# Kernel tuning notes

Hardware: AMD Instinct MI355X
Metric: run time of the kernel (lower is better)

Reference implementation:

```python
import jax, jax.numpy as jnp
import numpy as np

EPS = 0.001
NUM_HEAD = 4

def _bn(x, g, b, m, v):
    # x: [B,C,H,W]; per-channel affine batchnorm in eval mode
    inv = g / jnp.sqrt(v + EPS)
    return x * inv[None, :, None, None] + (b - m * inv)[None, :, None, None]

def setup_inputs() -> dict:
    key = jax.random.key(0)
    ks = jax.random.split(key, 16)
    B, C, H, W = 8, 256, 40, 40
    C2 = 2 * C
    return {
        "x": jax.random.normal(ks[0], (B, C, H, W), jnp.float32),
        "qkv_w": jax.random.normal(ks[1], (C2, C), jnp.float32) * 0.05,
        "qkv_g": jax.random.uniform(ks[2], (C2,), jnp.float32),
        "qkv_b": jax.random.normal(ks[3], (C2,), jnp.float32) * 0.05,
        "qkv_m": jax.random.normal(ks[4], (C2,), jnp.float32) * 0.05,
        "qkv_v": jax.random.uniform(ks[5], (C2,), jnp.float32) + 0.5,
        "cb1_w": jax.random.normal(ks[6], (C, 1, 3, 3), jnp.float32) * 0.05,
        "cb1_g": jax.random.uniform(ks[7], (C,), jnp.float32),
        "cb1_b": jax.random.normal(ks[8], (C,), jnp.float32) * 0.05,
        "cb1_m": jax.random.normal(ks[9], (C,), jnp.float32) * 0.05,
        "cb1_v": jax.random.uniform(ks[10], (C,), jnp.float32) + 0.5,
        "cb2_w": jax.random.normal(ks[11], (C, C), jnp.float32) * 0.05,
        "cb2_g": jax.random.uniform(ks[12], (C,), jnp.float32),
        "cb2_b": jax.random.normal(ks[13], (C,), jnp.float32) * 0.05,
        "cb2_m": jax.random.normal(ks[14], (C,), jnp.float32) * 0.05,
        "cb2_v": jax.random.uniform(ks[15], (C,), jnp.float32) + 0.5,
    }

def reference(x, qkv_w, qkv_g, qkv_b, qkv_m, qkv_v,
              cb1_w, cb1_g, cb1_b, cb1_m, cb1_v,
              cb2_w, cb2_g, cb2_b, cb2_m, cb2_v):
    B, C, H, W = x.shape
    nh = NUM_HEAD
    dh = C // nh          # dim_head
    dk = dh // 2          # dim_key
    scale = dk ** -0.5
    L = H * W

    # qkv: 1x1 conv (ch -> 2ch) + BN
    qkv = jnp.einsum('oc,bchw->bohw', qkv_w, x)
    qkv = _bn(qkv, qkv_g, qkv_b, qkv_m, qkv_v)
    qkv = qkv.reshape(B, nh, 2 * dk + dh, L)
    q, k, v = qkv[:, :, :dk], qkv[:, :, dk:2 * dk], qkv[:, :, 2 * dk:]

    # attn = q^T @ k * scale -> softmax over last dim
    attn = jnp.einsum('bndq,bndk->bnqk', q, k) * scale  # [B,nh,L,L]
    attn = jax.nn.softmax(attn, axis=-1)

    # y = v @ attn^T : y[d,q] = sum_k v[d,k] * attn[q,k]
    y = jnp.einsum('bndk,bnqk->bndq', v, attn).reshape(B, C, H, W)

    # depthwise 3x3 conv branch on v + BN
    vr = v.reshape(B, C, H, W)
    dw = jax.lax.conv_general_dilated(
        vr, cb1_w, window_strides=(1, 1), padding=((1, 1), (1, 1)),
        feature_group_count=C, dimension_numbers=('NCHW', 'OIHW', 'NCHW'))
    y = y + _bn(dw, cb1_g, cb1_b, cb1_m, cb1_v)

    # final 1x1 conv + BN
    out = jnp.einsum('oc,bchw->bohw', cb2_w, y)
    return _bn(out, cb2_g, cb2_b, cb2_m, cb2_v)
```

## Files before the change

kernel.cpp:

```cpp
#include <hip/hip_runtime.h>
#include <hip/hip_bf16.h>

#define EPS 1e-3f
#define QSC_LOG2E 0.2550348653f

typedef __attribute__((ext_vector_type(8))) short bf16x8;
typedef __attribute__((ext_vector_type(4))) float f32x4;
typedef __attribute__((ext_vector_type(4))) unsigned short u16x4;
typedef __attribute__((ext_vector_type(8))) unsigned short u16x8;
typedef __attribute__((ext_vector_type(2))) unsigned int u32x2;

typedef const __attribute__((address_space(1))) unsigned int g_u32;
typedef __attribute__((address_space(3))) unsigned int l_u32;

__device__ __forceinline__ unsigned short f2bf(float f) {
    union { float f; unsigned u; } v; v.f = f;
    unsigned r = v.u + 0x7FFFu + ((v.u >> 16) & 1u);
    return (unsigned short)(r >> 16);
}
__device__ __forceinline__ float bf2f(unsigned short h) {
    union { unsigned u; float f; } v; v.u = ((unsigned)h) << 16;
    return v.f;
}
__device__ __forceinline__ unsigned pkbf(float lo, float hi) {
    float2 t; t.x = lo; t.y = hi;
    __hip_bfloat162 h = __float22bfloat162_rn(t);
    union { __hip_bfloat162 h; unsigned u; } c; c.h = h;
    return c.u;
}

__global__ __launch_bounds__(256) void conv_kernel(
    const float* __restrict__ wq, const float* __restrict__ wc,
    unsigned short* __restrict__ wqb, unsigned short* __restrict__ wcb,
    const float* __restrict__ x, unsigned short* __restrict__ xt)
{
    int bid = blockIdx.x;
    int tid = threadIdx.x;
    if (bid < 192) {
        int i = (bid * 256 + tid) * 4;
        const float* src; unsigned short* dst; int off;
        if (i < 131072) { src = wq; dst = wqb; off = i; }
        else            { src = wc; dst = wcb; off = i - 131072; }
        f32x4 v = *(const f32x4*)(src + off);
        u16x4 o;
        #pragma unroll
        for (int j = 0; j < 4; ++j) o[j] = f2bf(v[j]);
        *(u16x4*)(dst + off) = o;
        return;
    }
    __shared__ float t[64][65];
    int bid2 = bid - 192;
    int l0 = (bid2 % 25) * 64, c0 = ((bid2 / 25) & 3) * 64, b = bid2 / 100;
    const float* xb = x + ((size_t)b * 256 + c0) * 1600 + l0;
    #pragma unroll
    for (int p = 0; p < 4; ++p) {
        int row = p * 16 + (tid >> 4);
        int col = (tid & 15) * 4;
        f32x4 v = *(const f32x4*)(xb + (size_t)row * 1600 + col);
        #pragma unroll
        for (int j = 0; j < 4; ++j) t[row][col + j] = v[j];
    }
    __syncthreads();
    int l = tid >> 2, cs = tid & 3;
    u16x8 o0, o1;
    #pragma unroll
    for (int i = 0; i < 8; ++i) o0[i] = f2bf(t[cs * 16 + i][l]);
    #pragma unroll
    for (int i = 0; i < 8; ++i) o1[i] = f2bf(t[cs * 16 + 8 + i][l]);
    unsigned short* dst = xt + ((size_t)b * 1600 + l0 + l) * 256 + c0 + cs * 16;
    *(u16x8*)dst = o0;
    *(u16x8*)(dst + 8) = o1;
}

__global__ __launch_bounds__(256) void qkv_gemm_kernel(
    const unsigned short* __restrict__ wqb, const unsigned short* __restrict__ xt,
    const float* __restrict__ gg, const float* __restrict__ bet,
    const float* __restrict__ mm, const float* __restrict__ vv,
    unsigned short* __restrict__ qk, unsigned short* __restrict__ vt,
    unsigned short* __restrict__ v2)
{
    __shared__ unsigned short ldsT[4][32 * 72];

    const int tid = threadIdx.x, wid = tid >> 6, lane = tid & 63;
    const int g = lane >> 4, cc = lane & 15;
    const int gl0 = blockIdx.x * 128 + (wid & 1) * 64;
    const int o_base = blockIdx.y * 64 + (wid >> 1) * 32;

    const unsigned short* wb0 = wqb + (size_t)(o_base + cc) * 256;
    const unsigned short* wb1 = wqb + (size_t)(o_base + 16 + cc) * 256;
    const unsigned short* xb  = xt + (size_t)(gl0 + cc) * 256;

    const f32x4 fz = {0.f, 0.f, 0.f, 0.f};
    f32x4 acc[2][4] = {{fz, fz, fz, fz}, {fz, fz, fz, fz}};
    #pragma unroll 4
    for (int kk = 0; kk < 256; kk += 32) {
        bf16x8 a0 = *(const bf16x8*)(wb0 + kk + 8 * g);
        bf16x8 a1 = *(const bf16x8*)(wb1 + kk + 8 * g);
        #pragma unroll
        for (int f = 0; f < 4; ++f) {
            bf16x8 bfr = *(const bf16x8*)(xb + (size_t)f * 16 * 256 + kk + 8 * g);
            acc[0][f] = __builtin_amdgcn_mfma_f32_16x16x32_bf16(a0, bfr, acc[0][f], 0, 0, 0);
            acc[1][f] = __builtin_amdgcn_mfma_f32_16x16x32_bf16(a1, bfr, acc[1][f], 0, 0, 0);
        }
    }

    const int head = blockIdx.y >> 1;
    const bool is_v = blockIdx.y & 1;
    float inv[2][4], bias[2][4];
    #pragma unroll
    for (int i = 0; i < 2; ++i) {
        #pragma unroll
        for (int r = 0; r < 4; ++r) {
            int oc = o_base + 16 * i + 4 * g + r;
            float iv = gg[oc] * rsqrtf(vv[oc] + EPS);
            float bs = bet[oc] - mm[oc] * iv;
            if ((oc & 127) < 32) { iv *= QSC_LOG2E; bs *= QSC_LOG2E; }
            inv[i][r] = iv; bias[i][r] = bs;
        }
    }

    if (!is_v) {
        #pragma unroll
        for (int f = 0; f < 4; ++f) {
            int gl = gl0 + 16 * f + cc;
            int b  = gl / 1600;
            int ll = gl - b * 1600;
            unsigned short* dst = qk + ((size_t)(b * 4 + head) * 1600 + ll) * 64;
            #pragma unroll
            for (int i = 0; i < 2; ++i) {
                u16x4 pk;
                #pragma unroll
                for (int r = 0; r < 4; ++r) pk[r] = f2bf(acc[i][f][r] * inv[i][r] + bias[i][r]);
                *(u16x4*)(dst + (o_base & 63) + 16 * i + 4 * g) = pk;
            }
        }
    } else {
        const int d_base = (o_base & 63);
        #pragma unroll
        for (int f = 0; f < 4; ++f) {
            int gl = gl0 + 16 * f + cc;
            unsigned short* v2dst = v2 + (size_t)gl * 256 + head * 64 + d_base;
            #pragma unroll
            for (int i = 0; i < 2; ++i) {
                u16x4 pk;
                #pragma unroll
                for (int r = 0; r < 4; ++r) {
                    unsigned short h = f2bf(acc[i][f][r] * inv[i][r] + bias[i][r]);
                    pk[r] = h;
                    ldsT[wid][(16 * i + 4 * g + r) * 72 + 16 * f + cc] = h;
                }
                *(u16x4*)(v2dst + 16 * i + 4 * g) = pk;
            }
        }
        asm volatile("s_waitcnt lgkmcnt(0)" ::: "memory");
        #pragma unroll
        for (int j = 0; j < 4; ++j) {
            int p = j * 64 + lane;
            int d_loc = p >> 3, c8 = p & 7;
            u16x8 val = *(const u16x8*)&ldsT[wid][d_loc * 72 + c8 * 8];
            int gl_c = gl0 + c8 * 8;
            int b  = gl_c / 1600;
            int ll = gl_c - b * 1600;
            *(u16x8*)(vt + ((size_t)(b * 4 + head) * 64 + d_base + d_loc) * 1600 + ll) = val;
        }
    }
}

__global__ __launch_bounds__(256) void attn_kernel(
    const unsigned short* __restrict__ qk, const unsigned short* __restrict__ vt,
    unsigned short* __restrict__ y_t)
{
    __shared__ __align__(16) unsigned short kbuf[2][64 * 32];
    __shared__ __align__(16) unsigned short vbuf[2][64 * 64];

    const int tid = threadIdx.x, wid = tid >> 6, lane = tid & 63;
    const int g = lane >> 4, cc = lane & 15;
    const int pair = blockIdx.x;
    const int q0 = blockIdx.y * 64 + wid * 16;

    const unsigned short* qkb = qk + (size_t)pair * 1600 * 64;
    const unsigned short* vtb = vt + (size_t)pair * 64 * 1600;

    bf16x8 bq = *(const bf16x8*)(qkb + (size_t)(q0 + cc) * 64 + 8 * g);

    const int krow = tid >> 2, kchk = tid & 3;
    const unsigned short* kP = qkb + (size_t)krow * 64 + 32 + (kchk ^ (krow & 3)) * 8;
    const int vrow = tid >> 3, vchk = tid & 7;
    const unsigned short* vPa = vtb + (size_t)vrow * 1600 + (vchk ^ (vrow & 7)) * 8;
    const unsigned short* vPb = vPa + (size_t)32 * 1600;

    const unsigned short* kr0  = &kbuf[0][cc * 32 + (g ^ (cc & 3)) * 8];
    const unsigned short* kr1  = &kbuf[1][cc * 32 + (g ^ (cc & 3)) * 8];
    const unsigned short* vr0a = &vbuf[0][cc * 64 + ((g) ^ (cc & 7)) * 8];
    const unsigned short* vr0b = &vbuf[0][cc * 64 + ((4 + g) ^ (cc & 7)) * 8];
    const unsigned short* vr1a = &vbuf[1][cc * 64 + ((g) ^ (cc & 7)) * 8];
    const unsigned short* vr1b = &vbuf[1][cc * 64 + ((4 + g) ^ (cc & 7)) * 8];

    #define STAGE(bufi)                                                               \
        do {                                                                          \
            __builtin_amdgcn_global_load_lds((g_u32*)kP,                              \
                (l_u32*)(&kbuf[bufi][wid * 512]), 16, 0, 0);                          \
            __builtin_amdgcn_global_load_lds((g_u32*)vPa,                             \
                (l_u32*)(&vbuf[bufi][wid * 512]), 16, 0, 0);                          \
            __builtin_amdgcn_global_load_lds((g_u32*)vPb,                             \
                (l_u32*)(&vbuf[bufi][2048 + wid * 512]), 16, 0, 0);                   \
            kP += 4096; vPa += 64; vPb += 64;                                         \
        } while (0)

    const f32x4 fz = {0.f, 0.f, 0.f, 0.f};
    const short one_bf = (short)0x3F80;
    const bf16x8 ones = {one_bf, one_bf, one_bf, one_bf, one_bf, one_bf, one_bf, one_bf};
    f32x4 o[4] = {fz, fz, fz, fz};
    f32x4 sumacc = fz;

    auto compute = [&](const unsigned short* kr, const unsigned short* vra,
                       const unsigned short* vrb) {
        bf16x8 kf[4], vf[8];
        #pragma unroll
        for (int f = 0; f < 4; ++f)
            kf[f] = *(const bf16x8*)(kr + f * 512);
        #pragma unroll
        for (int f2 = 0; f2 < 4; ++f2) {
            vf[2 * f2]     = *(const bf16x8*)(vra + f2 * 1024);
            vf[2 * f2 + 1] = *(const bf16x8*)(vrb + f2 * 1024);
        }

        f32x4 s4[4];
        __builtin_amdgcn_s_setprio(1);
        #pragma unroll
        for (int f = 0; f < 4; ++f)
            s4[f] = __builtin_amdgcn_mfma_f32_16x16x32_bf16(kf[f], bq, fz, 0, 0, 0);
        __builtin_amdgcn_s_setprio(0);

        unsigned c2[4][2];
        #pragma unroll
        for (int f = 0; f < 4; ++f) {
            float p0 = exp2f(s4[f][0]), p1 = exp2f(s4[f][1]);
            float p2 = exp2f(s4[f][2]), p3 = exp2f(s4[f][3]);
            c2[f][0] = pkbf(p0, p1);
            c2[f][1] = pkbf(p2, p3);
        }
        unsigned pb_u[2][4];
        #pragma unroll
        for (int s2 = 0; s2 < 2; ++s2) {
            const int fA = 2 * s2, fB = 2 * s2 + 1;
            u32x2 xy0 = __builtin_amdgcn_permlane32_swap(c2[fA][0], c2[fB][0], false, false);
            u32x2 xy1 = __builtin_amdgcn_permlane32_swap(c2[fA][1], c2[fB][1], false, false);
            u32x2 w02 = __builtin_amdgcn_permlane16_swap(xy0.x, xy0.y, false, false);
            u32x2 w13 = __builtin_amdgcn_permlane16_swap(xy1.x, xy1.y, false, false);
            pb_u[s2][0] = w02.x;
            pb_u[s2][1] = w13.x;
            pb_u[s2][2] = w02.y;
            pb_u[s2][3] = w13.y;
        }

        __builtin_amdgcn_s_setprio(1);
        #pragma unroll
        for (int s2 = 0; s2 < 2; ++s2) {
            union { unsigned u[4]; bf16x8 v; } pb;
            #pragma unroll
            for (int j = 0; j < 4; ++j) pb.u[j] = pb_u[s2][j];
            #pragma unroll
            for (int f2 = 0; f2 < 4; ++f2)
                o[f2] = __builtin_amdgcn_mfma_f32_16x16x32_bf16(vf[f2 * 2 + s2], pb.v, o[f2], 0, 0, 0);
            sumacc = __builtin_amdgcn_mfma_f32_16x16x32_bf16(ones, pb.v, sumacc, 0, 0, 0);
        }
        __builtin_amdgcn_s_setprio(0);
    };

    STAGE(0);
    __syncthreads();

    for (int j = 0; j < 12; ++j) {
        STAGE(1);
        compute(kr0, vr0a, vr0b);
        __syncthreads();
        STAGE(0);
        compute(kr1, vr1a, vr1b);
        __syncthreads();
    }
    compute(kr0, vr0a, vr0b);
    #undef STAGE

    float il = 1.f / sumacc[0];
    const int n = pair & 3, b = pair >> 2;
    unsigned short* yb = y_t + ((size_t)b * 1600 + q0 + cc) * 256 + n * 64;
    #pragma unroll
    for (int f2 = 0; f2 < 4; ++f2) {
        u16x4 st;
        #pragma unroll
        for (int r = 0; r < 4; ++r) st[r] = f2bf(o[f2][r] * il);
        *(u16x4*)(yb + 16 * f2 + 4 * g) = st;
    }
}

__global__ __launch_bounds__(256) void dw_kernel(
    const unsigned short* __restrict__ v2, unsigned short* __restrict__ y_t,
    const float* __restrict__ cw, const float* __restrict__ gg,
    const float* __restrict__ bet, const float* __restrict__ mm,
    const float* __restrict__ vv)
{
    const int tid = threadIdx.x;
    const int gl = blockIdx.x * 64 + (tid & 63);
    const int c0 = blockIdx.y * 32 + (tid >> 6) * 8;
    const int b = gl / 1600;
    const int l = gl - b * 1600;
    const int h = l / 40, w = l - h * 40;

    float s[8];
    #pragma unroll
    for (int i = 0; i < 8; ++i) s[i] = 0.f;
    #pragma unroll
    for (int kh = -1; kh <= 1; ++kh) {
        int hh = h + kh;
        if (hh < 0 || hh >= 40) continue;
        #pragma unroll
        for (int kw = -1; kw <= 1; ++kw) {
            int ww = w + kw;
            if (ww < 0 || ww >= 40) continue;
            u16x8 vv8 = *(const u16x8*)(v2 + (size_t)(gl + kh * 40 + kw) * 256 + c0);
            const int tap = (kh + 1) * 3 + (kw + 1);
            #pragma unroll
            for (int i = 0; i < 8; ++i)
                s[i] = fmaf(bf2f(vv8[i]), cw[(c0 + i) * 9 + tap], s[i]);
        }
    }
    u16x8 yv = *(const u16x8*)(y_t + (size_t)gl * 256 + c0);
    u16x8 out;
    #pragma unroll
    for (int i = 0; i < 8; ++i) {
        int c = c0 + i;
        float iv = gg[c] * rsqrtf(vv[c] + EPS);
        out[i] = f2bf(bf2f(yv[i]) + s[i] * iv + (bet[c] - mm[c] * iv));
    }
    *(u16x8*)(y_t + (size_t)gl * 256 + c0) = out;
}

__global__ __launch_bounds__(256) void out_gemm_kernel(
    const unsigned short* __restrict__ wcb, const unsigned short* __restrict__ y_t,
    const float* __restrict__ gg, const float* __restrict__ bet,
    const float* __restrict__ mm, const float* __restrict__ vv,
    float* __restrict__ out)
{
    const int tid = threadIdx.x, wid = tid >> 6, lane = tid & 63;
    const int g = lane >> 4, cc = lane & 15;
    const int gl0 = blockIdx.x * 128 + (wid & 1) * 64;
    const int o_base = blockIdx.y * 64 + (wid >> 1) * 32;

    const unsigned short* wb0 = wcb + (size_t)(o_base + cc) * 256;
    const unsigned short* wb1 = wcb + (size_t)(o_base + 16 + cc) * 256;
    const unsigned short* yb  = y_t + (size_t)(gl0 + cc) * 256;

    const f32x4 fz = {0.f, 0.f, 0.f, 0.f};
    f32x4 acc[2][4] = {{fz, fz, fz, fz}, {fz, fz, fz, fz}};
    #pragma unroll 4
    for (int kk = 0; kk < 256; kk += 32) {
        bf16x8 a0 = *(const bf16x8*)(wb0 + kk + 8 * g);
        bf16x8 a1 = *(const bf16x8*)(wb1 + kk + 8 * g);
        #pragma unroll
        for (int f = 0; f < 4; ++f) {
            bf16x8 bfr = *(const bf16x8*)(yb + (size_t)f * 16 * 256 + kk + 8 * g);
            acc[0][f] = __builtin_amdgcn_mfma_f32_16x16x32_bf16(a0, bfr, acc[0][f], 0, 0, 0);
            acc[1][f] = __builtin_amdgcn_mfma_f32_16x16x32_bf16(a1, bfr, acc[1][f], 0, 0, 0);
        }
    }
    #pragma unroll
    for (int i = 0; i < 2; ++i) {
        #pragma unroll
        for (int r = 0; r < 4; ++r) {
            int oc = o_base + 16 * i + 4 * g + r;
            float iv = gg[oc] * rsqrtf(vv[oc] + EPS);
            float bs = bet[oc] - mm[oc] * iv;
            #pragma unroll
            for (int f = 0; f < 4; ++f) {
                int gl = gl0 + 16 * f + cc;
                int b  = gl / 1600;
                int ll = gl - b * 1600;
                out[((size_t)b * 256 + oc) * 1600 + ll] = acc[i][f][r] * iv + bs;
            }
        }
    }
}

extern "C" void kernel_launch(void* const* d_in, const int* in_sizes, int n_in,
                              void* d_out, int out_size, void* d_ws, size_t ws_size,
                              hipStream_t stream) {
    const float* x     = (const float*)d_in[0];
    const float* qkv_w = (const float*)d_in[1];
    const float* qkv_g = (const float*)d_in[2];
    const float* qkv_b = (const float*)d_in[3];
    const float* qkv_m = (const float*)d_in[4];
    const float* qkv_v = (const float*)d_in[5];
    const float* cb1_w = (const float*)d_in[6];
    const float* cb1_g = (const float*)d_in[7];
    const float* cb1_b = (const float*)d_in[8];
    const float* cb1_m = (const float*)d_in[9];
    const float* cb1_v = (const float*)d_in[10];
    const float* cb2_w = (const float*)d_in[11];
    const float* cb2_g = (const float*)d_in[12];
    const float* cb2_b = (const float*)d_in[13];
    const float* cb2_m = (const float*)d_in[14];
    const float* cb2_v = (const float*)d_in[15];
    float* out = (float*)d_out;

    unsigned short* ws16 = (unsigned short*)d_ws;
    const size_t N16 = 3276800;
    unsigned short* xt  = ws16;
    unsigned short* qk  = ws16 + N16;
    unsigned short* vt  = ws16 + 2 * N16;
    unsigned short* y_t = ws16 + 3 * N16;
    unsigned short* v2  = ws16 + 4 * N16;
    unsigned short* wqb = ws16 + 5 * N16;
    unsigned short* wcb = wqb + 131072;

    conv_kernel<<<dim3(992), 256, 0, stream>>>(qkv_w, cb2_w, wqb, wcb, x, xt);
    qkv_gemm_kernel<<<dim3(100, 8), 256, 0, stream>>>(wqb, xt, qkv_g, qkv_b, qkv_m, qkv_v, qk, vt, v2);
    attn_kernel<<<dim3(32, 25), 256, 0, stream>>>(qk, vt, y_t);
    dw_kernel<<<dim3(200, 8), 256, 0, stream>>>(v2, y_t, cb1_w, cb1_g, cb1_b, cb1_m, cb1_v);
    out_gemm_kernel<<<dim3(100, 4), 256, 0, stream>>>(wcb, y_t, cb2_g, cb2_b, cb2_m, cb2_v, out);
}
```

Before: 118.7 us.

## Fuse depthwise conv into output GEMM via LDS and relax attention barriers

Merges the depthwise 3x3 conv + BN kernel with the final 1x1 conv GEMM. Each block computes 32 positions of the combined y into shared memory, then runs the MFMA GEMM across all 256 output channels. This drops one launch and the round trip of y_t through global memory. Separately, the attention loop's __syncthreads are replaced by explicit s_waitcnt vmcnt(3) plus raw barriers so prefetched loads can stay in flight across the barrier. The cost is a smaller grid (400 blocks), repeated weight reads per block, and a hand-tuned vmcnt that must match the number of loads STAGE issues.

```diff
diff --git a/kernel.cpp b/kernel.cpp
--- a/kernel.cpp
+++ b/kernel.cpp
@@ -269,16 +269,21 @@
     };
 
     STAGE(0);
-    __syncthreads();
 
     for (int j = 0; j < 12; ++j) {
         STAGE(1);
+        asm volatile("s_waitcnt vmcnt(3)" ::: "memory");
+        __builtin_amdgcn_s_barrier();
         compute(kr0, vr0a, vr0b);
-        __syncthreads();
+        __builtin_amdgcn_s_barrier();
         STAGE(0);
+        asm volatile("s_waitcnt vmcnt(3)" ::: "memory");
+        __builtin_amdgcn_s_barrier();
         compute(kr1, vr1a, vr1b);
-        __syncthreads();
-    }
+        __builtin_amdgcn_s_barrier();
+    }
+    asm volatile("s_waitcnt vmcnt(0)" ::: "memory");
+    __builtin_amdgcn_s_barrier();
     compute(kr0, vr0a, vr0b);
     #undef STAGE
 
@@ -294,85 +299,90 @@
     }
 }
 
-__global__ __launch_bounds__(256) void dw_kernel(
-    const unsigned short* __restrict__ v2, unsigned short* __restrict__ y_t,
-    const float* __restrict__ cw, const float* __restrict__ gg,
-    const float* __restrict__ bet, const float* __restrict__ mm,
-    const float* __restrict__ vv)
-{
-    const int tid = threadIdx.x;
-    const int gl = blockIdx.x * 64 + (tid & 63);
-    const int c0 = blockIdx.y * 32 + (tid >> 6) * 8;
-    const int b = gl / 1600;
-    const int l = gl - b * 1600;
-    const int h = l / 40, w = l - h * 40;
-
-    float s[8];
-    #pragma unroll
-    for (int i = 0; i < 8; ++i) s[i] = 0.f;
-    #pragma unroll
-    for (int kh = -1; kh <= 1; ++kh) {
-        int hh = h + kh;
-        if (hh < 0 || hh >= 40) continue;
-        #pragma unroll
-        for (int kw = -1; kw <= 1; ++kw) {
-            int ww = w + kw;
-            if (ww < 0 || ww >= 40) continue;
-            u16x8 vv8 = *(const u16x8*)(v2 + (size_t)(gl + kh * 40 + kw) * 256 + c0);
-            const int tap = (kh + 1) * 3 + (kw + 1);
-            #pragma unroll
-            for (int i = 0; i < 8; ++i)
-                s[i] = fmaf(bf2f(vv8[i]), cw[(c0 + i) * 9 + tap], s[i]);
-        }
-    }
-    u16x8 yv = *(const u16x8*)(y_t + (size_t)gl * 256 + c0);
-    u16x8 out;
-    #pragma unroll
-    for (int i = 0; i < 8; ++i) {
-        int c = c0 + i;
-        float iv = gg[c] * rsqrtf(vv[c] + EPS);
-        out[i] = f2bf(bf2f(yv[i]) + s[i] * iv + (bet[c] - mm[c] * iv));
-    }
-    *(u16x8*)(y_t + (size_t)gl * 256 + c0) = out;
-}
-
-__global__ __launch_bounds__(256) void out_gemm_kernel(
-    const unsigned short* __restrict__ wcb, const unsigned short* __restrict__ y_t,
-    const float* __restrict__ gg, const float* __restrict__ bet,
-    const float* __restrict__ mm, const float* __restrict__ vv,
+__global__ __launch_bounds__(256) void dwout_kernel(
+    const unsigned short* __restrict__ v2, const unsigned short* __restrict__ y_t,
+    const float* __restrict__ cw, const float* __restrict__ g1,
+    const float* __restrict__ b1, const float* __restrict__ m1,
+    const float* __restrict__ v1,
+    const unsigned short* __restrict__ wcb, const float* __restrict__ g2,
+    const float* __restrict__ b2, const float* __restrict__ m2,
+    const float* __restrict__ vbn2,
     float* __restrict__ out)
 {
+    __shared__ unsigned short y2s[32][264];
+
     const int tid = threadIdx.x, wid = tid >> 6, lane = tid & 63;
     const int g = lane >> 4, cc = lane & 15;
-    const int gl0 = blockIdx.x * 128 + (wid & 1) * 64;
-    const int o_base = blockIdx.y * 64 + (wid >> 1) * 32;
-
-    const unsigned short* wb0 = wcb + (size_t)(o_base + cc) * 256;
-    const unsigned short* wb1 = wcb + (size_t)(o_base + 16 + cc) * 256;
-    const unsigned short* yb  = y_t + (size_t)(gl0 + cc) * 256;
+    const int gl0 = blockIdx.x * 32;
+
+    {
+        const int gl_loc = tid & 31, cpart = tid >> 5;
+        const int gl = gl0 + gl_loc;
+        const int b = gl / 1600, l = gl - b * 1600;
+        const int h = l / 40, w = l - h * 40;
+        #pragma unroll
+        for (int cg = 0; cg < 4; ++cg) {
+            const int c0 = cpart * 32 + cg * 8;
+            float s[8];
+            #pragma unroll
+            for (int i = 0; i < 8; ++i) s[i] = 0.f;
+            #pragma unroll
+            for (int kh = -1; kh <= 1; ++kh) {
+                int hh = h + kh;
+                if (hh < 0 || hh >= 40) continue;
+                #pragma unroll
+                for (int kw = -1; kw <= 1; ++kw) {
+                    int ww = w + kw;
+                    if (ww < 0 || ww >= 40) continue;
+                    u16x8 vv8 = *(const u16x8*)(v2 + (size_t)(gl + kh * 40 + kw) * 256 + c0);
+                    const int tap = (kh + 1) * 3 + (kw + 1);
+                    #pragma unroll
+                    for (int i = 0; i < 8; ++i)
+                        s[i] = fmaf(bf2f(vv8[i]), cw[(c0 + i) * 9 + tap], s[i]);
+                }
+            }
+            u16x8 yv = *(const u16x8*)(y_t + (size_t)gl * 256 + c0);
+            u16x8 o8;
+            #pragma unroll
+            for (int i = 0; i < 8; ++i) {
+                int c = c0 + i;
+                float iv = g1[c] * rsqrtf(v1[c] + EPS);
+                o8[i] = f2bf(bf2f(yv[i]) + s[i] * iv + (b1[c] - m1[c] * iv));
+            }
+            *(u16x8*)&y2s[gl_loc][c0] = o8;
+        }
+    }
+    __syncthreads();
+
+    const int o_base = wid * 64;
+    const unsigned short* wb = wcb + (size_t)(o_base + cc) * 256;
 
     const f32x4 fz = {0.f, 0.f, 0.f, 0.f};
-    f32x4 acc[2][4] = {{fz, fz, fz, fz}, {fz, fz, fz, fz}};
+    f32x4 acc[4][2] = {{fz, fz}, {fz, fz}, {fz, fz}, {fz, fz}};
     #pragma unroll 4
     for (int kk = 0; kk < 256; kk += 32) {
-        bf16x8 a0 = *(const bf16x8*)(wb0 + kk + 8 * g);
-        bf16x8 a1 = *(const bf16x8*)(wb1 + kk + 8 * g);
-        #pragma unroll
-        for (int f = 0; f < 4; ++f) {
-            bf16x8 bfr = *(const bf16x8*)(yb + (size_t)f * 16 * 256 + kk + 8 * g);
-            acc[0][f] = __builtin_amdgcn_mfma_f32_16x16x32_bf16(a0, bfr, acc[0][f], 0, 0, 0);
-            acc[1][f] = __builtin_amdgcn_mfma_f32_16x16x32_bf16(a1, bfr, acc[1][f], 0, 0, 0);
-        }
-    }
-    #pragma unroll
-    for (int i = 0; i < 2; ++i) {
+        bf16x8 a[4], bfr[2];
+        #pragma unroll
+        for (int i = 0; i < 4; ++i)
+            a[i] = *(const bf16x8*)(wb + (size_t)i * 16 * 256 + kk + 8 * g);
+        #pragma unroll
+        for (int f = 0; f < 2; ++f)
+            bfr[f] = *(const bf16x8*)&y2s[16 * f + cc][kk + 8 * g];
+        #pragma unroll
+        for (int i = 0; i < 4; ++i)
+            #pragma unroll
+            for (int f = 0; f < 2; ++f)
+                acc[i][f] = __builtin_amdgcn_mfma_f32_16x16x32_bf16(a[i], bfr[f], acc[i][f], 0, 0, 0);
+    }
+    #pragma unroll
+    for (int i = 0; i < 4; ++i) {
         #pragma unroll
         for (int r = 0; r < 4; ++r) {
             int oc = o_base + 16 * i + 4 * g + r;
-            float iv = gg[oc] * rsqrtf(vv[oc] + EPS);
-            float bs = bet[oc] - mm[oc] * iv;
-            #pragma unroll
-            for (int f = 0; f < 4; ++f) {
+            float iv = g2[oc] * rsqrtf(vbn2[oc] + EPS);
+            float bs = b2[oc] - m2[oc] * iv;
+            #pragma unroll
+            for (int f = 0; f < 2; ++f) {
                 int gl = gl0 + 16 * f + cc;
                 int b  = gl / 1600;
                 int ll = gl - b * 1600;
@@ -416,6 +426,6 @@
     conv_kernel<<<dim3(992), 256, 0, stream>>>(qkv_w, cb2_w, wqb, wcb, x, xt);
     qkv_gemm_kernel<<<dim3(100, 8), 256, 0, stream>>>(wqb, xt, qkv_g, qkv_b, qkv_m, qkv_v, qk, vt, v2);
     attn_kernel<<<dim3(32, 25), 256, 0, stream>>>(qk, vt, y_t);
-    dw_kernel<<<dim3(200, 8), 256, 0, stream>>>(v2, y_t, cb1_w, cb1_g, cb1_b, cb1_m, cb1_v);
-    out_gemm_kernel<<<dim3(100, 4), 256, 0, stream>>>(wcb, y_t, cb2_g, cb2_b, cb2_m, cb2_v, out);
-}
+    dwout_kernel<<<dim3(400), 256, 0, stream>>>(v2, y_t, cb1_w, cb1_g, cb1_b, cb1_m, cb1_v,
+                                                wcb, cb2_g, cb2_b, cb2_m, cb2_v, out);
+}
```

Result: faster. 114.0 us (-4.0%).
